# Performance work log

Measured on AMD Instinct MI355X. Metric: run time of the kernel, lower is better.

Reference implementation:

```python
import jax, jax.numpy as jnp
import numpy as np

# PyTorch LSTM gate order: i, f, g, o. Bidirectional LSTM with hidden = dim/2,
# outputs concatenated -> dim, then mean over the sequence axis (as in the module).

def _lstm_dir(x, Wih, Whh, bih, bhh):
    # x: [B, T, D] -> hidden states [B, T, H]
    B, T, _ = x.shape
    H = Whh.shape[1]
    gx = jnp.einsum('btd,gd->btg', x, Wih) + bih + bhh  # precompute input gates [B,T,4H]
    def step(carry, g_t):
        h, c = carry
        g = g_t + h @ Whh.T
        i, f, gg, o = jnp.split(g, 4, axis=-1)
        c = jax.nn.sigmoid(f) * c + jax.nn.sigmoid(i) * jnp.tanh(gg)
        h = jax.nn.sigmoid(o) * jnp.tanh(c)
        return (h, c), h
    z = jnp.zeros((B, H), x.dtype)
    _, hs = jax.lax.scan(step, (z, z), jnp.swapaxes(gx, 0, 1))
    return jnp.swapaxes(hs, 0, 1)


def _bilstm_mean(x, Wih, Whh, bih, bhh):
    # params indexed [dir, ...]; dir 0 = forward, dir 1 = backward.
    hf = _lstm_dir(x, Wih[0], Whh[0], bih[0], bhh[0])
    hb = _lstm_dir(x[:, ::-1], Wih[1], Whh[1], bih[1], bhh[1])[:, ::-1]
    return jnp.concatenate([hf, hb], axis=-1).mean(axis=1)  # [B, 2H] == [B, D]


def setup_inputs() -> dict:
    key = jax.random.key(0)
    ks = jax.random.split(key, 14)
    N, C, D, K, H = 30000, 3, 128, 10, 64
    f = lambda k, shp: jax.random.normal(k, shp, jnp.float32) * 0.1
    return dict(
        x_a=f(ks[0], (N, C, D)),
        x_b=f(ks[1], (N, C, D)),
        x_c=f(ks[2], (N, C, D)),
        Wih_c=f(ks[3], (2, 4 * H, D)),
        Whh_c=f(ks[4], (2, 4 * H, H)),
        bih_c=f(ks[5], (2, 4 * H)),
        bhh_c=f(ks[6], (2, 4 * H)),
        Wih_n=f(ks[7], (3, 2, 4 * H, D)),
        Whh_n=f(ks[8], (3, 2, 4 * H, H)),
        bih_n=f(ks[9], (3, 2, 4 * H)),
        bhh_n=f(ks[10], (3, 2, 4 * H)),
        attn_w=f(ks[11], (3, 2 * D)),
        attn_b=f(ks[12], (3,)),
        nbr_idx=jax.random.randint(ks[13], (3, 3, N, K), 0, N),  # [stype, dtype, N, K]
    )


def reference(x_a, x_b, x_c, Wih_c, Whh_c, bih_c, bhh_c,
              Wih_n, Whh_n, bih_n, bhh_n, attn_w, attn_b, nbr_idx):
    xs = [x_a, x_b, x_c]
    NT = 3
    # C2: heterogeneous content encoder (shared bi-LSTM over content features)
    content = [_bilstm_mean(x, Wih_c, Whh_c, bih_c, bhh_c) for x in xs]  # each [N, D]
    out = []
    for d in range(NT):
        # C3: per-source-type neighbor aggregation via that stype's bi-LSTM reducer
        neighs = []
        for s in range(NT):
            msgs = content[s][nbr_idx[s, d]]  # mailbox gather [N, K, D]
            neighs.append(_bilstm_mean(msgs, Wih_n[s], Whh_n[s], bih_n[s], bhh_n[s]))
        d_h = content[d]
        emd = jnp.stack(neighs + [d_h], axis=1)  # [N, 4, D]
        ch = jnp.concatenate(
            [jnp.broadcast_to(d_h[:, None, :], emd.shape), emd], axis=-1)  # [N, 4, 2D]
        logits = jax.nn.leaky_relu(
            jnp.einsum('nkf,f->nk', ch, attn_w[d]) + attn_b[d], 0.01)
        w = jax.nn.softmax(logits, axis=1)  # [N, 4]
        out.append(jnp.einsum('nk,nkd->nd', w, emd))  # attention-weighted fusion
    return tuple(out)
```

## Files before the change

### kernel.cpp

```cpp
#include <hip/hip_runtime.h>

#define N_NODES 30000
#define DFEAT 128
#define HID 64
#define G4 256

typedef __bf16 bfrag __attribute__((ext_vector_type(8)));
typedef float f32x4 __attribute__((ext_vector_type(4)));

__device__ inline float bflo(unsigned u){ return __builtin_bit_cast(float, u << 16); }
__device__ inline float bfhi(unsigned u){ return __builtin_bit_cast(float, u & 0xFFFF0000u); }
__device__ inline unsigned short bf16u(float a){
  unsigned ua = __builtin_bit_cast(unsigned, a);
  ua += 0x7FFFu + ((ua >> 16) & 1u);
  return (unsigned short)(ua >> 16);
}
__device__ inline unsigned packbf(float a, float b){
  unsigned ua = __builtin_bit_cast(unsigned, a);
  unsigned ub = __builtin_bit_cast(unsigned, b);
  ua += 0x7FFFu + ((ua >> 16) & 1u);
  ub += 0x7FFFu + ((ub >> 16) & 1u);
  return (ua >> 16) | (ub & 0xFFFF0000u);
}
__device__ inline float sigm(float x){
  float e = __builtin_amdgcn_exp2f(-1.442695041f * x);
  return __builtin_amdgcn_rcpf(1.f + e);
}
__device__ inline float tanh_(float x){
  float e = __builtin_amdgcn_exp2f(-2.885390082f * x);
  return __builtin_amdgcn_rcpf(1.f + e) * 2.f - 1.f;
}
__device__ inline bfrag ldfrag(const unsigned short* p){
  return *reinterpret_cast<const bfrag*>(p);
}
__device__ inline f32x4 mfma16(bfrag a, bfrag b, f32x4 c){
  return __builtin_amdgcn_mfma_f32_16x16x32_bf16(a, b, c, 0, 0, 0);
}
__device__ inline int idx_stride(const int* p){
  int lane = threadIdx.x & 63;
  int v = p[lane];
  int ok = (lane & 1) ? (v == 0) : (v >= 0 && v < N_NODES);
  unsigned long long m = __ballot(ok);
  int st = (m == ~0ull) ? 2 : 1;
  return __builtin_amdgcn_readfirstlane(st);
}

#define PK_WHHC 65536
#define PK_WIHN 98304
#define PK_WHHN 294912

__global__ __launch_bounds__(256) void k_pack(
    const float* __restrict__ Wih_c, const float* __restrict__ Whh_c,
    const float* __restrict__ Wih_n, const float* __restrict__ Whh_n,
    unsigned short* __restrict__ pk)
{
  const int m = blockIdx.y;
  const float* src; unsigned short* dst; int ndir, Q;
  if (m == 0){ src = Wih_c; dst = pk;            ndir = 2; Q = 4; }
  else if (m == 1){ src = Whh_c; dst = pk + PK_WHHC; ndir = 2; Q = 2; }
  else if (m == 2){ src = Wih_n; dst = pk + PK_WIHN; ndir = 6; Q = 4; }
  else { src = Whh_n; dst = pk + PK_WHHN; ndir = 6; Q = 2; }
  const int per = Q * 8192;
  const int total = ndir * per;
  int e = blockIdx.x * 256 + threadIdx.x;
  if (e >= total) return;
  int sd = e / per, r = e % per;
  int c = r / (Q * 2048); int r2 = r % (Q * 2048);
  int q = r2 / 2048;      int r3 = r2 % 2048;
  int w = r3 >> 9; int lane = (r3 >> 3) & 63; int j = r3 & 7;
  int gate = c * 64 + w * 16 + (lane & 15);
  int col  = q * 32 + (lane >> 4) * 8 + j;
  int D = Q * 32;
  dst[e] = bf16u(src[((size_t)sd * G4 + gate) * D + col]);
}

__global__ __launch_bounds__(256) void k_content(
    const float* __restrict__ xa, const float* __restrict__ xb,
    const float* __restrict__ xc,
    const unsigned short* __restrict__ pk,
    const float* __restrict__ bih, const float* __restrict__ bhh,
    unsigned short* __restrict__ content)
{
  const int tile = blockIdx.x, dir = blockIdx.y, s = blockIdx.z;
  const float* xs = (s == 0) ? xa : ((s == 1) ? xb : xc);
  const int n0 = tile * 16;
  __shared__ __align__(16) unsigned int xdw[48 * 68];
  __shared__ __align__(16) unsigned short hbuf[2][16 * 72];
  const int tid = threadIdx.x;
  const float2* xg2 = reinterpret_cast<const float2*>(xs + (size_t)n0 * 384);
  for (int i = tid; i < 3072; i += 256){
    int node = i / 192, rem = i % 192; int t = rem / 64, c2 = rem % 64;
    float2 v = xg2[i];
    xdw[(t * 16 + node) * 68 + c2] = packbf(v.x, v.y);
  }
  for (int i = tid; i < 1152; i += 256) hbuf[0][i] = 0;

  const int lane = tid & 63, w = tid >> 6;
  const int nl = lane & 15, kg = lane >> 4;
  const unsigned short* pkWih = pk + dir * 32768;
  const unsigned short* pkWhh = pk + PK_WHHC + dir * 16384;
  bfrag Bw[4][4], Bh[4][2];
  float bias[4];
  #pragma unroll
  for (int c = 0; c < 4; ++c){
    int gate = c * 64 + w * 16 + nl;
    #pragma unroll
    for (int q = 0; q < 4; ++q)
      Bw[c][q] = ldfrag(pkWih + (((c * 4 + q) * 4 + w) * 64 + lane) * 8);
    Bh[c][0] = ldfrag(pkWhh + (((c * 2 + 0) * 4 + w) * 64 + lane) * 8);
    Bh[c][1] = ldfrag(pkWhh + (((c * 2 + 1) * 4 + w) * 64 + lane) * 8);
    bias[c] = bih[dir * G4 + gate] + bhh[dir * G4 + gate];
  }
  __syncthreads();

  float cst[4] = {0,0,0,0}, hsum[4] = {0,0,0,0};
  int pp = 0;
  for (int t = 0; t < 3; ++t){
    int tt = dir ? (2 - t) : t;
    f32x4 acc[4];
    #pragma unroll
    for (int c = 0; c < 4; ++c){ f32x4 bv = {bias[c], bias[c], bias[c], bias[c]}; acc[c] = bv; }
    const unsigned short* xrow = reinterpret_cast<const unsigned short*>(&xdw[(tt * 16 + nl) * 68]);
    bfrag ax[4];
    #pragma unroll
    for (int q = 0; q < 4; ++q) ax[q] = ldfrag(xrow + q * 32 + kg * 8);
    #pragma unroll
    for (int c = 0; c < 4; ++c){
      #pragma unroll
      for (int q = 0; q < 4; ++q) acc[c] = mfma16(ax[q], Bw[c][q], acc[c]);
    }
    const unsigned short* hrow = &hbuf[pp][nl * 72];
    bfrag ah0 = ldfrag(hrow + kg * 8);
    bfrag ah1 = ldfrag(hrow + 32 + kg * 8);
    #pragma unroll
    for (int c = 0; c < 4; ++c){
      acc[c] = mfma16(ah0, Bh[c][0], acc[c]);
      acc[c] = mfma16(ah1, Bh[c][1], acc[c]);
    }
    #pragma unroll
    for (int r = 0; r < 4; ++r){
      float gi = acc[0][r], gf = acc[1][r], gg = acc[2][r], go = acc[3][r];
      float cn = sigm(gf) * cst[r] + sigm(gi) * tanh_(gg);
      cst[r] = cn;
      float h = sigm(go) * tanh_(cn);
      hsum[r] += h;
      hbuf[pp ^ 1][(kg * 4 + r) * 72 + (w * 16 + nl)] = bf16u(h);
    }
    __syncthreads();
    pp ^= 1;
  }
  #pragma unroll
  for (int r = 0; r < 4; ++r){
    int n = n0 + kg * 4 + r;
    content[((size_t)s * N_NODES + n) * DFEAT + dir * 64 + w * 16 + nl] = bf16u(hsum[r] * (1.f / 3.f));
  }
}

__global__ __launch_bounds__(256) void k_gtab(
    const unsigned short* __restrict__ content,
    const unsigned short* __restrict__ pk,
    const float* __restrict__ bih_n, const float* __restrict__ bhh_n,
    unsigned int* __restrict__ Gtab)
{
  const int tile = blockIdx.x, dir = blockIdx.y, s = blockIdx.z;
  const int n0 = tile * 16;
  __shared__ __align__(16) unsigned int cdw[16 * 68];
  const int tid = threadIdx.x;
  const unsigned int* cg = reinterpret_cast<const unsigned int*>(content) + ((size_t)s * N_NODES + n0) * 64;
  for (int i = tid; i < 1024; i += 256){
    int node = i >> 6, c2 = i & 63;
    cdw[node * 68 + c2] = cg[i];
  }
  __syncthreads();
  const int lane = tid & 63, w = tid >> 6;
  const int nl = lane & 15, kg = lane >> 4;
  const int sd = s * 2 + dir;
  const unsigned short* pkW = pk + PK_WIHN + sd * 32768;
  f32x4 acc[4];
  #pragma unroll
  for (int c = 0; c < 4; ++c){
    int gate = c * 64 + w * 16 + nl;
    float b = bih_n[sd * G4 + gate] + bhh_n[sd * G4 + gate];
    f32x4 bv = {b, b, b, b};
    acc[c] = bv;
  }
  const unsigned short* crow = reinterpret_cast<const unsigned short*>(&cdw[nl * 68]);
  bfrag a[4];
  #pragma unroll
  for (int q = 0; q < 4; ++q) a[q] = ldfrag(crow + q * 32 + kg * 8);
  #pragma unroll
  for (int c = 0; c < 4; ++c){
    #pragma unroll
    for (int q = 0; q < 4; ++q){
      bfrag bw = ldfrag(pkW + (((c * 4 + q) * 4 + w) * 64 + lane) * 8);
      acc[c] = mfma16(a[q], bw, acc[c]);
    }
  }
  uint2* g2 = reinterpret_cast<uint2*>(Gtab + (size_t)sd * N_NODES * 128);
  #pragma unroll
  for (int r = 0; r < 4; ++r){
    int n = n0 + kg * 4 + r;
    uint2 v;
    v.x = packbf(acc[0][r], acc[1][r]);
    v.y = packbf(acc[2][r], acc[3][r]);
    g2[(size_t)n * 64 + (w * 16 + nl)] = v;
  }
}

__global__ __launch_bounds__(256, 4) void k_neigh(
    const unsigned int* __restrict__ Gtab,
    const unsigned short* __restrict__ pk,
    const int* __restrict__ nbr_idx,
    int d,
    unsigned short* __restrict__ nbuf)
{
  const int tile = blockIdx.x, dir = blockIdx.y, s = blockIdx.z;
  const int n0 = tile * 16;
  __shared__ int idxb[160];
  __shared__ __align__(16) unsigned short hbuf[2][16 * 72];
  const int tid = threadIdx.x;
  const int st = idx_stride(nbr_idx);
  const size_t ibase = ((size_t)(s * 3 + d) * N_NODES + n0) * 10;
  if (tid < 160) idxb[tid] = nbr_idx[(ibase + tid) * st];
  for (int i = tid; i < 1152; i += 256) hbuf[0][i] = 0;
  __syncthreads();
  const int lane = tid & 63, w = tid >> 6;
  const int nl = lane & 15, kg = lane >> 4;
  const int sd = s * 2 + dir;
  const unsigned short* pkW = pk + PK_WHHN + sd * 16384;
  bfrag Bh[4][2];
  #pragma unroll
  for (int c = 0; c < 4; ++c){
    Bh[c][0] = ldfrag(pkW + (((c * 2 + 0) * 4 + w) * 64 + lane) * 8);
    Bh[c][1] = ldfrag(pkW + (((c * 2 + 1) * 4 + w) * 64 + lane) * 8);
  }
  const uint2* gt2 = reinterpret_cast<const uint2*>(Gtab + (size_t)sd * N_NODES * 128);
  uint2 gn[4];
  {
    int ke = dir ? 9 : 0;
    #pragma unroll
    for (int r = 0; r < 4; ++r){
      int ridx = idxb[(kg * 4 + r) * 10 + ke];
      gn[r] = gt2[(size_t)ridx * 64 + (w * 16 + nl)];
    }
  }
  float cst[4] = {0,0,0,0}, hsum[4] = {0,0,0,0};
  int pp = 0;
  for (int t = 0; t < 10; ++t){
    uint2 cur[4];
    #pragma unroll
    for (int r = 0; r < 4; ++r) cur[r] = gn[r];
    if (t < 9){
      int ke = dir ? (8 - t) : (t + 1);
      #pragma unroll
      for (int r = 0; r < 4; ++r){
        int ridx = idxb[(kg * 4 + r) * 10 + ke];
        gn[r] = gt2[(size_t)ridx * 64 + (w * 16 + nl)];
      }
    }
    f32x4 acc[4];
    #pragma unroll
    for (int r = 0; r < 4; ++r){
      acc[0][r] = bflo(cur[r].x); acc[1][r] = bfhi(cur[r].x);
      acc[2][r] = bflo(cur[r].y); acc[3][r] = bfhi(cur[r].y);
    }
    const unsigned short* hrow = &hbuf[pp][nl * 72];
    bfrag ah0 = ldfrag(hrow + kg * 8);
    bfrag ah1 = ldfrag(hrow + 32 + kg * 8);
    #pragma unroll
    for (int c = 0; c < 4; ++c){
      acc[c] = mfma16(ah0, Bh[c][0], acc[c]);
      acc[c] = mfma16(ah1, Bh[c][1], acc[c]);
    }
    #pragma unroll
    for (int r = 0; r < 4; ++r){
      float gi = acc[0][r], gf = acc[1][r], gg = acc[2][r], go = acc[3][r];
      float cn = sigm(gf) * cst[r] + sigm(gi) * tanh_(gg);
      cst[r] = cn;
      float h = sigm(go) * tanh_(cn);
      hsum[r] += h;
      hbuf[pp ^ 1][(kg * 4 + r) * 72 + (w * 16 + nl)] = bf16u(h);
    }
    __syncthreads();
    pp ^= 1;
  }
  #pragma unroll
  for (int r = 0; r < 4; ++r){
    int n = n0 + kg * 4 + r;
    nbuf[((size_t)s * N_NODES + n) * DFEAT + dir * 64 + w * 16 + nl] = bf16u(hsum[r] * 0.1f);
  }
}

__global__ __launch_bounds__(256) void k_attn(
    const unsigned short* __restrict__ content,
    const unsigned short* __restrict__ nbuf,
    const float* __restrict__ attn_w,
    const float* __restrict__ attn_b,
    int d,
    float* __restrict__ out)
{
  const int n = blockIdx.x * 4 + (threadIdx.x >> 6);
  const int lane = threadIdx.x & 63;
  const unsigned int* dh = reinterpret_cast<const unsigned int*>(content) + ((size_t)d * N_NODES + n) * 64;
  const float2* awv = reinterpret_cast<const float2*>(attn_w + d * 256);
  unsigned int udh = dh[lane];
  unsigned int ue[3];
  #pragma unroll
  for (int s_ = 0; s_ < 3; ++s_){
    const unsigned int* np_ = reinterpret_cast<const unsigned int*>(nbuf) + ((size_t)s_ * N_NODES + n) * 64;
    ue[s_] = np_[lane];
  }
  float2 wl = awv[lane], wh = awv[64 + lane];
  float dh0 = bflo(udh), dh1 = bfhi(udh);
  float p[5];
  p[4] = wl.x * dh0 + wl.y * dh1;
  #pragma unroll
  for (int k = 0; k < 3; ++k){
    p[k] = wh.x * bflo(ue[k]) + wh.y * bfhi(ue[k]);
  }
  p[3] = wh.x * dh0 + wh.y * dh1;
  #pragma unroll
  for (int m = 1; m < 64; m <<= 1){
    #pragma unroll
    for (int jj = 0; jj < 5; ++jj) p[jj] += __shfl_xor(p[jj], m, 64);
  }
  float bias = attn_b[d];
  float logit[4];
  #pragma unroll
  for (int k = 0; k < 4; ++k){
    float x = p[4] + p[k] + bias;
    logit[k] = x > 0.f ? x : 0.01f * x;
  }
  float mx = fmaxf(fmaxf(logit[0], logit[1]), fmaxf(logit[2], logit[3]));
  float ek[4], Z = 0.f;
  #pragma unroll
  for (int k = 0; k < 4; ++k){ ek[k] = __builtin_amdgcn_exp2f(1.442695041f * (logit[k] - mx)); Z += ek[k]; }
  float rz = __builtin_amdgcn_rcpf(Z);
  float o0 = 0.f, o1 = 0.f;
  #pragma unroll
  for (int k = 0; k < 3; ++k){
    float wk = ek[k] * rz;
    o0 += wk * bflo(ue[k]); o1 += wk * bfhi(ue[k]);
  }
  float w3 = ek[3] * rz;
  o0 += w3 * dh0; o1 += w3 * dh1;
  float2 res; res.x = o0; res.y = o1;
  reinterpret_cast<float2*>(out)[((size_t)d * N_NODES + n) * 64 + lane] = res;
}

extern "C" void kernel_launch(void* const* d_in, const int* in_sizes, int n_in,
                              void* d_out, int out_size, void* d_ws, size_t ws_size,
                              hipStream_t stream)
{
  const float* xa    = (const float*)d_in[0];
  const float* xb    = (const float*)d_in[1];
  const float* xc    = (const float*)d_in[2];
  const float* Wih_c = (const float*)d_in[3];
  const float* Whh_c = (const float*)d_in[4];
  const float* bih_c = (const float*)d_in[5];
  const float* bhh_c = (const float*)d_in[6];
  const float* Wih_n = (const float*)d_in[7];
  const float* Whh_n = (const float*)d_in[8];
  const float* bih_n = (const float*)d_in[9];
  const float* bhh_n = (const float*)d_in[10];
  const float* attn_w = (const float*)d_in[11];
  const float* attn_b = (const float*)d_in[12];
  const int*   nbr   = (const int*)d_in[13];
  float* out = (float*)d_out;

  char* ws = (char*)d_ws;
  unsigned short* content = (unsigned short*)ws;
  unsigned int*   Gtab    = (unsigned int*)(ws + 23040000);
  unsigned short* nbuf    = (unsigned short*)(ws + 115200000);
  unsigned short* pkw     = (unsigned short*)(ws + 138240000);

  k_pack<<<dim3(768, 4), 256, 0, stream>>>(Wih_c, Whh_c, Wih_n, Whh_n, pkw);
  k_content<<<dim3(1875, 2, 3), 256, 0, stream>>>(xa, xb, xc, pkw, bih_c, bhh_c, content);
  k_gtab<<<dim3(1875, 2, 3), 256, 0, stream>>>(content, pkw, bih_n, bhh_n, Gtab);
  for (int d = 0; d < 3; ++d){
    k_neigh<<<dim3(1875, 2, 3), 256, 0, stream>>>(Gtab, pkw, nbr, d, nbuf);
    k_attn<<<dim3(7500), 256, 0, stream>>>(content, nbuf, attn_w, attn_b, d, out);
  }
}
```

Before: 892.8 us.

## Fold activation scales into packed weights and merge LSTM gate reciprocals

Pre-scales the packed LSTM weights and biases by -log2(e) (sigmoid gates) or -2log2(e) (tanh gate), so the gate pre-activations feed exp2 directly. The cell update then combines the sigmoid and tanh reciprocals into one rcp per product, cutting transcendental and multiply work in the serial recurrence. It also replaces the manual bf16 rounding with the hardware conversion, precomputes neighbor row offsets, and fully unrolls the time loops. In exchange, rounding the scaled weights to bf16 changes numerics slightly, and the exp products could overflow for large inputs.

```diff
diff --git a/kernel.cpp b/kernel.cpp
--- a/kernel.cpp
+++ b/kernel.cpp
@@ -7,6 +7,9 @@
 
 typedef __bf16 bfrag __attribute__((ext_vector_type(8)));
 typedef float f32x4 __attribute__((ext_vector_type(4)));
+
+#define SC_SIG -1.442695041f
+#define SC_TANH -2.885390082f
 
 __device__ inline float bflo(unsigned u){ return __builtin_bit_cast(float, u << 16); }
 __device__ inline float bfhi(unsigned u){ return __builtin_bit_cast(float, u & 0xFFFF0000u); }
@@ -15,20 +18,15 @@
   ua += 0x7FFFu + ((ua >> 16) & 1u);
   return (unsigned short)(ua >> 16);
 }
+__device__ inline unsigned short bfn(float a){
+  return __builtin_bit_cast(unsigned short, (__bf16)a);
+}
 __device__ inline unsigned packbf(float a, float b){
   unsigned ua = __builtin_bit_cast(unsigned, a);
   unsigned ub = __builtin_bit_cast(unsigned, b);
   ua += 0x7FFFu + ((ua >> 16) & 1u);
   ub += 0x7FFFu + ((ub >> 16) & 1u);
   return (ua >> 16) | (ub & 0xFFFF0000u);
-}
-__device__ inline float sigm(float x){
-  float e = __builtin_amdgcn_exp2f(-1.442695041f * x);
-  return __builtin_amdgcn_rcpf(1.f + e);
-}
-__device__ inline float tanh_(float x){
-  float e = __builtin_amdgcn_exp2f(-2.885390082f * x);
-  return __builtin_amdgcn_rcpf(1.f + e) * 2.f - 1.f;
 }
 __device__ inline bfrag ldfrag(const unsigned short* p){
   return *reinterpret_cast<const bfrag*>(p);
@@ -43,6 +41,22 @@
   unsigned long long m = __ballot(ok);
   int st = (m == ~0ull) ? 2 : 1;
   return __builtin_amdgcn_readfirstlane(st);
+}
+
+__device__ inline float lstm_step(float gi, float gf, float gg, float go,
+                                  float& cst, float& hsum)
+{
+  float ei = __builtin_amdgcn_exp2f(gi);
+  float ef = __builtin_amdgcn_exp2f(gf);
+  float eg = __builtin_amdgcn_exp2f(gg);
+  float cn = cst * __builtin_amdgcn_rcpf(1.f + ef)
+           + (1.f - eg) * __builtin_amdgcn_rcpf((1.f + ei) * (1.f + eg));
+  cst = cn;
+  float eo = __builtin_amdgcn_exp2f(go);
+  float ec = __builtin_amdgcn_exp2f(SC_TANH * cn);
+  float h = (1.f - ec) * __builtin_amdgcn_rcpf((1.f + eo) * (1.f + ec));
+  hsum += h;
+  return h;
 }
 
 #define PK_WHHC 65536
@@ -71,7 +85,8 @@
   int gate = c * 64 + w * 16 + (lane & 15);
   int col  = q * 32 + (lane >> 4) * 8 + j;
   int D = Q * 32;
-  dst[e] = bf16u(src[((size_t)sd * G4 + gate) * D + col]);
+  float sc = (c == 2) ? SC_TANH : SC_SIG;
+  dst[e] = bf16u(src[((size_t)sd * G4 + gate) * D + col] * sc);
 }
 
 __global__ __launch_bounds__(256) void k_content(
@@ -109,12 +124,14 @@
       Bw[c][q] = ldfrag(pkWih + (((c * 4 + q) * 4 + w) * 64 + lane) * 8);
     Bh[c][0] = ldfrag(pkWhh + (((c * 2 + 0) * 4 + w) * 64 + lane) * 8);
     Bh[c][1] = ldfrag(pkWhh + (((c * 2 + 1) * 4 + w) * 64 + lane) * 8);
-    bias[c] = bih[dir * G4 + gate] + bhh[dir * G4 + gate];
+    float sc = (c == 2) ? SC_TANH : SC_SIG;
+    bias[c] = (bih[dir * G4 + gate] + bhh[dir * G4 + gate]) * sc;
   }
   __syncthreads();
 
   float cst[4] = {0,0,0,0}, hsum[4] = {0,0,0,0};
   int pp = 0;
+  #pragma unroll
   for (int t = 0; t < 3; ++t){
     int tt = dir ? (2 - t) : t;
     f32x4 acc[4];
@@ -139,12 +156,8 @@
     }
     #pragma unroll
     for (int r = 0; r < 4; ++r){
-      float gi = acc[0][r], gf = acc[1][r], gg = acc[2][r], go = acc[3][r];
-      float cn = sigm(gf) * cst[r] + sigm(gi) * tanh_(gg);
-      cst[r] = cn;
-      float h = sigm(go) * tanh_(cn);
-      hsum[r] += h;
-      hbuf[pp ^ 1][(kg * 4 + r) * 72 + (w * 16 + nl)] = bf16u(h);
+      float h = lstm_step(acc[0][r], acc[1][r], acc[2][r], acc[3][r], cst[r], hsum[r]);
+      hbuf[pp ^ 1][(kg * 4 + r) * 72 + (w * 16 + nl)] = bfn(h);
     }
     __syncthreads();
     pp ^= 1;
@@ -152,7 +165,7 @@
   #pragma unroll
   for (int r = 0; r < 4; ++r){
     int n = n0 + kg * 4 + r;
-    content[((size_t)s * N_NODES + n) * DFEAT + dir * 64 + w * 16 + nl] = bf16u(hsum[r] * (1.f / 3.f));
+    content[((size_t)s * N_NODES + n) * DFEAT + dir * 64 + w * 16 + nl] = bfn(hsum[r] * (1.f / 3.f));
   }
 }
 
@@ -180,7 +193,8 @@
   #pragma unroll
   for (int c = 0; c < 4; ++c){
     int gate = c * 64 + w * 16 + nl;
-    float b = bih_n[sd * G4 + gate] + bhh_n[sd * G4 + gate];
+    float sc = (c == 2) ? SC_TANH : SC_SIG;
+    float b = (bih_n[sd * G4 + gate] + bhh_n[sd * G4 + gate]) * sc;
     f32x4 bv = {b, b, b, b};
     acc[c] = bv;
   }
@@ -221,11 +235,12 @@
   const int tid = threadIdx.x;
   const int st = idx_stride(nbr_idx);
   const size_t ibase = ((size_t)(s * 3 + d) * N_NODES + n0) * 10;
-  if (tid < 160) idxb[tid] = nbr_idx[(ibase + tid) * st];
+  if (tid < 160) idxb[tid] = nbr_idx[(ibase + tid) * st] * 64;
   for (int i = tid; i < 1152; i += 256) hbuf[0][i] = 0;
   __syncthreads();
   const int lane = tid & 63, w = tid >> 6;
   const int nl = lane & 15, kg = lane >> 4;
+  const int lo = w * 16 + nl;
   const int sd = s * 2 + dir;
   const unsigned short* pkW = pk + PK_WHHN + sd * 16384;
   bfrag Bh[4][2];
@@ -240,12 +255,13 @@
     int ke = dir ? 9 : 0;
     #pragma unroll
     for (int r = 0; r < 4; ++r){
-      int ridx = idxb[(kg * 4 + r) * 10 + ke];
-      gn[r] = gt2[(size_t)ridx * 64 + (w * 16 + nl)];
+      unsigned off = (unsigned)idxb[(kg * 4 + r) * 10 + ke] + lo;
+      gn[r] = gt2[off];
     }
   }
   float cst[4] = {0,0,0,0}, hsum[4] = {0,0,0,0};
   int pp = 0;
+  #pragma unroll
   for (int t = 0; t < 10; ++t){
     uint2 cur[4];
     #pragma unroll
@@ -254,8 +270,8 @@
       int ke = dir ? (8 - t) : (t + 1);
       #pragma unroll
       for (int r = 0; r < 4; ++r){
-        int ridx = idxb[(kg * 4 + r) * 10 + ke];
-        gn[r] = gt2[(size_t)ridx * 64 + (w * 16 + nl)];
+        unsigned off = (unsigned)idxb[(kg * 4 + r) * 10 + ke] + lo;
+        gn[r] = gt2[off];
       }
     }
     f32x4 acc[4];
@@ -274,12 +290,8 @@
     }
     #pragma unroll
     for (int r = 0; r < 4; ++r){
-      float gi = acc[0][r], gf = acc[1][r], gg = acc[2][r], go = acc[3][r];
-      float cn = sigm(gf) * cst[r] + sigm(gi) * tanh_(gg);
-      cst[r] = cn;
-      float h = sigm(go) * tanh_(cn);
-      hsum[r] += h;
-      hbuf[pp ^ 1][(kg * 4 + r) * 72 + (w * 16 + nl)] = bf16u(h);
+      float h = lstm_step(acc[0][r], acc[1][r], acc[2][r], acc[3][r], cst[r], hsum[r]);
+      hbuf[pp ^ 1][(kg * 4 + r) * 72 + (w * 16 + nl)] = bfn(h);
     }
     __syncthreads();
     pp ^= 1;
@@ -287,7 +299,7 @@
   #pragma unroll
   for (int r = 0; r < 4; ++r){
     int n = n0 + kg * 4 + r;
-    nbuf[((size_t)s * N_NODES + n) * DFEAT + dir * 64 + w * 16 + nl] = bf16u(hsum[r] * 0.1f);
+    nbuf[((size_t)s * N_NODES + n) * DFEAT + dir * 64 + w * 16 + nl] = bfn(hsum[r] * 0.1f);
   }
 }
 
```

After: 872.0 us. 1.02x faster.
